# Kernel tuning notes

Measured on AMD Instinct MI355X. Metric: run time of the kernel, lower is better.

Reference implementation:

```python
import jax, jax.numpy as jnp
import numpy as np

B, D_CAT, C_IN, C_OUT, K, H, W = 16, 512, 256, 256, 3, 64, 64


def setup_inputs() -> dict:
    key = jax.random.key(0)
    ks = jax.random.split(key, 9)
    inp = {
        "x": jax.random.normal(ks[0], (B, C_IN, H, W), dtype=jnp.float32),
        "y": jax.random.normal(ks[1], (B, D_CAT), dtype=jnp.float32),
        # EqualLinear stack: d_catin -> in_channels, then n_dl=2 layers in_channels -> in_channels
        "w0": jax.random.normal(ks[2], (C_IN, D_CAT), dtype=jnp.float32) / np.sqrt(D_CAT),
        "b0": jnp.zeros((C_IN,), dtype=jnp.float32),
        "w1": jax.random.normal(ks[3], (C_IN, C_IN), dtype=jnp.float32) / np.sqrt(C_IN),
        "b1": jnp.zeros((C_IN,), dtype=jnp.float32),
        "w2": jax.random.normal(ks[4], (C_IN, C_IN), dtype=jnp.float32) / np.sqrt(C_IN),
        "b2": jnp.zeros((C_IN,), dtype=jnp.float32),
        # shared conv weight (O, I, k, k), modulated per sample
        "conv_w": jax.random.normal(ks[5], (C_OUT, C_IN, K, K), dtype=jnp.float32) / np.sqrt(C_IN * K * K),
    }
    return inp


def _lrelu(z):
    # nn.LeakyReLU default negative_slope = 0.01
    return jnp.where(z >= 0, z, 0.01 * z)


def reference(x, y, w0, b0, w1, b1, w2, b2, conv_w):
    # style MLP (EqualLinear stack with LeakyReLU)
    s = _lrelu(y @ w0.T + b0)          # (B, C_in)
    s = _lrelu(s @ w1.T + b1)
    s = _lrelu(s @ w2.T + b2)
    # Per-sample weight modulation: conv(x[b], W * s[b, None, :, None, None]).
    # Since the scale is per input channel (no demodulation), this is exactly
    # equivalent to scaling the input channels and running one shared conv —
    # the fused form a custom kernel would use.
    x_mod = x * s[:, :, None, None]    # (B, C_in, H, W)
    out = jax.lax.conv_general_dilated(
        x_mod, conv_w,
        window_strides=(1, 1),
        padding=((1, 1), (1, 1)),
        dimension_numbers=("NCHW", "OIHW", "NCHW"),
    )  # (B, C_out, H, W); conv has bias=False in _DyConv
    return out
```

## Files before the change

### kernel.cpp

```cpp
#include <hip/hip_runtime.h>

typedef short bf16x8 __attribute__((ext_vector_type(8)));
typedef float f32x4 __attribute__((ext_vector_type(4)));
typedef unsigned short ushort8 __attribute__((ext_vector_type(8)));
typedef unsigned short ushort4v __attribute__((ext_vector_type(4)));

#define BATCH 16
#define DCAT 512
#define CIN 256
#define COUT 256
#define HH 64
#define WW 64
#define HP 66
#define WP 66
#define PLANE (HP * WP * 8)

__device__ __forceinline__ unsigned short f2bf(float f) {
  unsigned int u = __float_as_uint(f);
  unsigned int r = (u + 0x7fffu + ((u >> 16) & 1u)) >> 16;
  return (unsigned short)r;
}

template <int IN_DIM>
__global__ void __launch_bounds__(256) mlp_layer(const float* __restrict__ in,
                                                 const float* __restrict__ w,
                                                 const float* __restrict__ bias,
                                                 float* __restrict__ out) {
  int wid = threadIdx.x >> 6, lane = threadIdx.x & 63;
  int oidx = blockIdx.x * 4 + wid;
  int b = oidx >> 8, c = oidx & 255;
  const float* wr = w + (size_t)c * IN_DIM;
  const float* ir = in + (size_t)b * IN_DIM;
  float sum = 0.f;
#pragma unroll
  for (int d0 = 0; d0 < IN_DIM; d0 += 256) {
    f32x4 wv = *(const f32x4*)(wr + d0 + lane * 4);
    f32x4 iv = *(const f32x4*)(ir + d0 + lane * 4);
    sum += wv[0] * iv[0] + wv[1] * iv[1] + wv[2] * iv[2] + wv[3] * iv[3];
  }
#pragma unroll
  for (int off = 32; off; off >>= 1) sum += __shfl_xor(sum, off, 64);
  if (lane == 0) {
    float a = sum + bias[c];
    out[oidx] = a >= 0.f ? a : 0.01f * a;
  }
}

__global__ void __launch_bounds__(256) prep_all(const float* __restrict__ t1,
                                                const float* __restrict__ w2,
                                                const float* __restrict__ b2,
                                                const float* __restrict__ x,
                                                const float* __restrict__ cw,
                                                unsigned short* __restrict__ xpad,
                                                unsigned short* __restrict__ wt) {
  int blk = blockIdx.x;
  int tid = threadIdx.x;

  if (blk >= 1024) {
    int idx = (blk - 1024) * 256 + tid;
    int t = idx / 16384;
    int r = idx - t * 16384;
    int o = r >> 6, i4 = r & 63;
    ushort4v v;
#pragma unroll
    for (int j = 0; j < 4; j++) v[j] = f2bf(cw[(o * 256 + i4 * 4 + j) * 9 + t]);
    *(ushort4v*)(wt + ((size_t)(t * COUT + o)) * CIN + i4 * 4) = v;
    return;
  }

  int h = blk & 1, c8 = (blk >> 1) & 31, b = blk >> 6;
  int wid = tid >> 6, lane = tid & 63;

  float tv = t1[b * CIN + tid];
  float pj[8];
#pragma unroll
  for (int j = 0; j < 8; j++) pj[j] = w2[(size_t)(c8 * 8 + j) * CIN + tid] * tv;

  const float* xb = x + ((size_t)(b * CIN + c8 * 8)) * (HH * WW);
  int gg0 = h * 512 + tid;
  int gg1 = gg0 + 256;
  int hh0 = (gg0 >> 4) + 1, w00 = (gg0 & 15) * 4 + 1;
  int hh1 = (gg1 >> 4) + 1, w01 = (gg1 & 15) * 4 + 1;
  int base0 = (hh0 - 1) * WW + (w00 - 1);
  int base1 = (hh1 - 1) * WW + (w01 - 1);
  f32x4 v0[8], v1[8];
#pragma unroll
  for (int j = 0; j < 8; j++) v0[j] = *(const f32x4*)(xb + j * (HH * WW) + base0);
#pragma unroll
  for (int j = 0; j < 8; j++) v1[j] = *(const f32x4*)(xb + j * (HH * WW) + base1);

#pragma unroll
  for (int off = 32; off; off >>= 1)
#pragma unroll
    for (int j = 0; j < 8; j++) pj[j] += __shfl_xor(pj[j], off, 64);
  __shared__ float red[4][8];
  __shared__ float sv_sh[8];
  if (lane == 0)
#pragma unroll
    for (int j = 0; j < 8; j++) red[wid][j] = pj[j];
  __syncthreads();
  if (tid < 8) {
    float a = red[0][tid] + red[1][tid] + red[2][tid] + red[3][tid] + b2[c8 * 8 + tid];
    sv_sh[tid] = a >= 0.f ? a : 0.01f * a;
  }
  __syncthreads();
  float sv[8];
#pragma unroll
  for (int j = 0; j < 8; j++) sv[j] = sv_sh[j];

  unsigned short* xp = xpad + ((size_t)(b * 32 + c8)) * PLANE;

  if (tid < 130) {
    int i = h * 130 + tid;
    int bh, bw;
    if (i < 66) { bh = 0; bw = i; }
    else if (i < 132) { bh = 65; bw = i - 66; }
    else if (i < 196) { bh = i - 132 + 1; bw = 0; }
    else { bh = i - 196 + 1; bw = 65; }
    ushort8 z = {0, 0, 0, 0, 0, 0, 0, 0};
    *(ushort8*)(xp + (bh * WP + bw) * 8) = z;
  }

  unsigned short* op0 = xp + (hh0 * WP + w00) * 8;
  unsigned short* op1 = xp + (hh1 * WP + w01) * 8;
#pragma unroll
  for (int t2 = 0; t2 < 4; t2++) {
    ushort8 o;
#pragma unroll
    for (int j = 0; j < 8; j++) o[j] = f2bf(v0[j][t2] * sv[j]);
    *(ushort8*)(op0 + t2 * 8) = o;
  }
#pragma unroll
  for (int t2 = 0; t2 < 4; t2++) {
    ushort8 o;
#pragma unroll
    for (int j = 0; j < 8; j++) o[j] = f2bf(v1[j][t2] * sv[j]);
    *(ushort8*)(op1 + t2 * 8) = o;
  }
}

__device__ __forceinline__ void gl2lds16(const void* g, void* l) {
  __builtin_amdgcn_global_load_lds((const __attribute__((address_space(1))) void*)g,
                                   (__attribute__((address_space(3))) void*)l, 16, 0, 0);
}

__global__ void __launch_bounds__(512, 1) gemm_conv(const unsigned short* __restrict__ xpad,
                                                    const unsigned short* __restrict__ wt,
                                                    float* __restrict__ out) {
  __shared__ __align__(16) char lds[131072];
  int tid = threadIdx.x;
  int wid = tid >> 6, lane = tid & 63;
  int bid = blockIdx.x;
  int m_t = (bid & 7) * 32 + (bid >> 3);
  int m0 = m_t << 8;
  int b = m0 >> 12;
  int h0 = (m0 >> 6) & 63;
  int wm = wid & 1, wn = wid >> 1;

  f32x4 acc[8][4];
#pragma unroll
  for (int mi = 0; mi < 8; mi++)
#pragma unroll
    for (int ni = 0; ni < 4; ni++) acc[mi][ni] = (f32x4){0.f, 0.f, 0.f, 0.f};

  int p = tid >> 3;
  int cs = tid & 7;
  int gs = cs ^ (p & 7);
  const unsigned short* aSt =
      xpad + ((size_t)((b * 32 + gs) * HP + h0)) * (WP * 8) + p * 8;
  const unsigned short* bSt = wt + (size_t)p * CIN + gs * 8;
  int dstOff = wid * 1024;

  int qa = lane >> 4;
  int rA = wm * 128 + (lane & 15);
  int rB = wn * 64 + (lane & 15);
  int offA0 = rA * 128 + ((qa ^ (lane & 7)) * 16);
  int offA1 = rA * 128 + (((qa + 4) ^ (lane & 7)) * 16);
  int offB0 = 65536 + rB * 128 + ((qa ^ (lane & 7)) * 16);
  int offB1 = 65536 + rB * 128 + (((qa + 4) ^ (lane & 7)) * 16);

#define STAGE(bo)                                       \
  do {                                                  \
    char* dA = lds + (bo) + dstOff;                     \
    char* dB = lds + 65536 + (bo) + dstOff;             \
    gl2lds16(aSt, dA);                                  \
    gl2lds16(aSt + WP * 8, dA + 8192);                  \
    gl2lds16(aSt + 2 * WP * 8, dA + 16384);             \
    gl2lds16(aSt + 3 * WP * 8, dA + 24576);             \
    gl2lds16(bSt, dB);                                  \
    gl2lds16(bSt + 64 * CIN, dB + 8192);                \
    gl2lds16(bSt + 128 * CIN, dB + 16384);              \
    gl2lds16(bSt + 192 * CIN, dB + 24576);              \
  } while (0)

  STAGE(0);
  aSt += 8 * PLANE;
  bSt += 64;
  __syncthreads();

  int bo = 0;
  for (int s = 0; s < 36; s++) {
    if (s < 35) {
      STAGE(bo ^ 32768);
      int sn = s + 1;
      if ((sn & 3) != 3) {
        aSt += 8 * PLANE;
        bSt += 64;
      } else {
        int tapn = sn >> 2;
        aSt += (tapn % 3 != 2) ? (8 - 24 * PLANE) : ((WP - 2) * 8 - 24 * PLANE);
        bSt += COUT * CIN - 192;
      }
    }

    const char* Ab = lds + bo;
#pragma unroll
    for (int kb = 0; kb < 2; kb++) {
      int oa = kb ? offA1 : offA0;
      int ob = kb ? offB1 : offB0;
      bf16x8 av[8], bv[4];
#pragma unroll
      for (int mi = 0; mi < 8; mi++)
        av[mi] = *(const bf16x8*)(Ab + oa + mi * 2048);
#pragma unroll
      for (int ni = 0; ni < 4; ni++)
        bv[ni] = *(const bf16x8*)(Ab + ob + ni * 2048);
#pragma unroll
      for (int mi = 0; mi < 8; mi++)
#pragma unroll
        for (int ni = 0; ni < 4; ni++)
          acc[mi][ni] = __builtin_amdgcn_mfma_f32_16x16x32_bf16(av[mi], bv[ni],
                                                                acc[mi][ni], 0, 0, 0);
    }

    __syncthreads();
    bo ^= 32768;
  }
#undef STAGE

  int pixbase = m0 & 4095;
  int quad = lane >> 4;
  int col = lane & 15;
#pragma unroll
  for (int mi = 0; mi < 8; mi++) {
    int pm = pixbase + wm * 128 + mi * 16 + quad * 4;
#pragma unroll
    for (int ni = 0; ni < 4; ni++) {
      int on = wn * 64 + ni * 16 + col;
      float* op = out + ((size_t)(b * COUT + on) << 12) + pm;
      *(f32x4*)op = acc[mi][ni];
    }
  }
}

extern "C" void kernel_launch(void* const* d_in, const int* in_sizes, int n_in,
                              void* d_out, int out_size, void* d_ws, size_t ws_size,
                              hipStream_t stream) {
  const float* x = (const float*)d_in[0];
  const float* y = (const float*)d_in[1];
  const float* w0 = (const float*)d_in[2];
  const float* b0 = (const float*)d_in[3];
  const float* w1 = (const float*)d_in[4];
  const float* b1 = (const float*)d_in[5];
  const float* w2 = (const float*)d_in[6];
  const float* b2 = (const float*)d_in[7];
  const float* cw = (const float*)d_in[8];
  float* out = (float*)d_out;

  char* ws = (char*)d_ws;
  float* t0 = (float*)ws;
  float* t1 = (float*)(ws + 16384);
  unsigned short* wt = (unsigned short*)(ws + 32768);
  unsigned short* xpad = (unsigned short*)(ws + 32768 + 9 * COUT * CIN * 2);

  mlp_layer<DCAT><<<BATCH * CIN / 4, 256, 0, stream>>>(y, w0, b0, t0);
  mlp_layer<CIN><<<BATCH * CIN / 4, 256, 0, stream>>>(t0, w1, b1, t1);
  prep_all<<<1024 + 576, 256, 0, stream>>>(t1, w2, b2, x, cw, xpad, wt);
  gemm_conv<<<BATCH * HH * WW / 256, 512, 0, stream>>>(xpad, wt, out);
}
```

Before: 209.3 us.

## Interleave LDS reads, async global-to-LDS loads and MFMA clusters with setprio

Restructures the main GEMM loop into four phases, each interleaving a batch of LDS fragment reads, two async global-to-LDS prefetches for the next stage, a barrier, and a 4x4 MFMA cluster wrapped in s_setprio. It replaces the single __syncthreads per stage with explicit vmcnt/lgkmcnt waits and raw s_barrier, and peels the last iteration. The aim is to overlap memory traffic with matrix math and reduce stall time at stage boundaries. The cost is more barriers per stage and fragile hand-placed waits that depend on exact load counts being correct.

```diff
diff --git a/kernel.cpp b/kernel.cpp
--- a/kernel.cpp
+++ b/kernel.cpp
@@ -143,6 +143,32 @@
   __builtin_amdgcn_global_load_lds((const __attribute__((address_space(1))) void*)g,
                                    (__attribute__((address_space(3))) void*)l, 16, 0, 0);
 }
+
+#define RD_AV(DST, OFF)                                   \
+  _Pragma("unroll")                                       \
+  for (int mi = 0; mi < 4; mi++)                          \
+    DST[mi] = *(const bf16x8*)(Ab + (OFF) + mi * 2048);
+
+#define RD_BV(DST, OFF)                                   \
+  _Pragma("unroll")                                       \
+  for (int ni = 0; ni < 4; ni++)                          \
+    DST[ni] = *(const bf16x8*)(Bb + (OFF) + ni * 2048);
+
+#define CLUSTER(MB, AV, BV)                                                 \
+  do {                                                                      \
+    __builtin_amdgcn_s_setprio(1);                                          \
+    _Pragma("unroll")                                                       \
+    for (int mi = 0; mi < 4; mi++)                                          \
+      _Pragma("unroll")                                                     \
+      for (int ni = 0; ni < 4; ni++)                                        \
+        acc[(MB) + mi][ni] = __builtin_amdgcn_mfma_f32_16x16x32_bf16(       \
+            AV[mi], BV[ni], acc[(MB) + mi][ni], 0, 0, 0);                   \
+    __builtin_amdgcn_s_setprio(0);                                          \
+  } while (0)
+
+#define WAIT_LGKM0()                                        \
+  asm volatile("s_waitcnt lgkmcnt(0)" ::: "memory");        \
+  __builtin_amdgcn_sched_barrier(0)
 
 __global__ void __launch_bounds__(512, 1) gemm_conv(const unsigned short* __restrict__ xpad,
                                                     const unsigned short* __restrict__ wt,
@@ -176,67 +202,95 @@
   int rB = wn * 64 + (lane & 15);
   int offA0 = rA * 128 + ((qa ^ (lane & 7)) * 16);
   int offA1 = rA * 128 + (((qa + 4) ^ (lane & 7)) * 16);
-  int offB0 = 65536 + rB * 128 + ((qa ^ (lane & 7)) * 16);
-  int offB1 = 65536 + rB * 128 + (((qa + 4) ^ (lane & 7)) * 16);
-
-#define STAGE(bo)                                       \
-  do {                                                  \
-    char* dA = lds + (bo) + dstOff;                     \
-    char* dB = lds + 65536 + (bo) + dstOff;             \
-    gl2lds16(aSt, dA);                                  \
-    gl2lds16(aSt + WP * 8, dA + 8192);                  \
-    gl2lds16(aSt + 2 * WP * 8, dA + 16384);             \
-    gl2lds16(aSt + 3 * WP * 8, dA + 24576);             \
-    gl2lds16(bSt, dB);                                  \
-    gl2lds16(bSt + 64 * CIN, dB + 8192);                \
-    gl2lds16(bSt + 128 * CIN, dB + 16384);              \
-    gl2lds16(bSt + 192 * CIN, dB + 24576);              \
-  } while (0)
-
-  STAGE(0);
+  int offB0 = rB * 128 + ((qa ^ (lane & 7)) * 16);
+  int offB1 = rB * 128 + (((qa + 4) ^ (lane & 7)) * 16);
+
+  {
+    char* dA = lds + dstOff;
+    char* dB = lds + 65536 + dstOff;
+    gl2lds16(aSt, dA);
+    gl2lds16(aSt + WP * 8, dA + 8192);
+    gl2lds16(aSt + 2 * WP * 8, dA + 16384);
+    gl2lds16(aSt + 3 * WP * 8, dA + 24576);
+    gl2lds16(bSt, dB);
+    gl2lds16(bSt + 64 * CIN, dB + 8192);
+    gl2lds16(bSt + 128 * CIN, dB + 16384);
+    gl2lds16(bSt + 192 * CIN, dB + 24576);
+  }
   aSt += 8 * PLANE;
   bSt += 64;
-  __syncthreads();
+  asm volatile("s_waitcnt vmcnt(0)" ::: "memory");
+  __builtin_amdgcn_s_barrier();
 
   int bo = 0;
-  for (int s = 0; s < 36; s++) {
-    if (s < 35) {
-      STAGE(bo ^ 32768);
-      int sn = s + 1;
-      if ((sn & 3) != 3) {
-        aSt += 8 * PLANE;
-        bSt += 64;
-      } else {
-        int tapn = sn >> 2;
-        aSt += (tapn % 3 != 2) ? (8 - 24 * PLANE) : ((WP - 2) * 8 - 24 * PLANE);
-        bSt += COUT * CIN - 192;
-      }
+  for (int s = 0; s < 35; s++) {
+    const char* Ab = lds + bo;
+    const char* Bb = lds + 65536 + bo;
+    char* dA = lds + (bo ^ 32768) + dstOff;
+    char* dB = lds + 65536 + (bo ^ 32768) + dstOff;
+    bf16x8 av[4], bv[4], aw[4], av2[4], bw[4], aw2[4];
+
+    RD_AV(av, offA0);
+    RD_BV(bv, offB0);
+    gl2lds16(bSt, dB);
+    gl2lds16(bSt + 64 * CIN, dB + 8192);
+    asm volatile("s_waitcnt vmcnt(2)" ::: "memory");
+    __builtin_amdgcn_s_barrier();
+    WAIT_LGKM0();
+    CLUSTER(0, av, bv);
+
+    RD_AV(aw, offA0 + 8192);
+    gl2lds16(bSt + 128 * CIN, dB + 16384);
+    gl2lds16(bSt + 192 * CIN, dB + 24576);
+    __builtin_amdgcn_s_barrier();
+    WAIT_LGKM0();
+    CLUSTER(4, aw, bv);
+
+    RD_AV(av2, offA1);
+    RD_BV(bw, offB1);
+    gl2lds16(aSt, dA);
+    gl2lds16(aSt + 2 * WP * 8, dA + 16384);
+    __builtin_amdgcn_s_barrier();
+    WAIT_LGKM0();
+    CLUSTER(0, av2, bw);
+
+    RD_AV(aw2, offA1 + 8192);
+    gl2lds16(aSt + WP * 8, dA + 8192);
+    gl2lds16(aSt + 3 * WP * 8, dA + 24576);
+    asm volatile("s_waitcnt vmcnt(2)" ::: "memory");
+    __builtin_amdgcn_s_barrier();
+    WAIT_LGKM0();
+    CLUSTER(4, aw2, bw);
+
+    int sn = s + 1;
+    if ((sn & 3) != 3) {
+      aSt += 8 * PLANE;
+      bSt += 64;
+    } else {
+      int tapn = sn >> 2;
+      aSt += (tapn % 3 != 2) ? (8 - 24 * PLANE) : ((WP - 2) * 8 - 24 * PLANE);
+      bSt += COUT * CIN - 192;
     }
-
+    bo ^= 32768;
+  }
+
+  {
     const char* Ab = lds + bo;
-#pragma unroll
-    for (int kb = 0; kb < 2; kb++) {
-      int oa = kb ? offA1 : offA0;
-      int ob = kb ? offB1 : offB0;
-      bf16x8 av[8], bv[4];
-#pragma unroll
-      for (int mi = 0; mi < 8; mi++)
-        av[mi] = *(const bf16x8*)(Ab + oa + mi * 2048);
-#pragma unroll
-      for (int ni = 0; ni < 4; ni++)
-        bv[ni] = *(const bf16x8*)(Ab + ob + ni * 2048);
-#pragma unroll
-      for (int mi = 0; mi < 8; mi++)
-#pragma unroll
-        for (int ni = 0; ni < 4; ni++)
-          acc[mi][ni] = __builtin_amdgcn_mfma_f32_16x16x32_bf16(av[mi], bv[ni],
-                                                                acc[mi][ni], 0, 0, 0);
-    }
-
-    __syncthreads();
-    bo ^= 32768;
-  }
-#undef STAGE
+    const char* Bb = lds + 65536 + bo;
+    asm volatile("s_waitcnt vmcnt(0)" ::: "memory");
+    __builtin_amdgcn_s_barrier();
+    bf16x8 av[4], bv[4];
+    RD_AV(av, offA0);
+    RD_BV(bv, offB0);
+    CLUSTER(0, av, bv);
+    RD_AV(av, offA0 + 8192);
+    CLUSTER(4, av, bv);
+    RD_AV(av, offA1);
+    RD_BV(bv, offB1);
+    CLUSTER(0, av, bv);
+    RD_AV(av, offA1 + 8192);
+    CLUSTER(4, av, bv);
+  }
 
   int pixbase = m0 & 4095;
   int quad = lane >> 4;
```

New measurement: 203.0 us. 1.03x faster.
